# Performance work log

Hardware: AMD Instinct MI355X
Metric: run time of the kernel (lower is better)

## Reference

```python
import jax, jax.numpy as jnp
import numpy as np

M, NN, D, H, DFF, L, EPG = 128, 62, 512, 8, 2048, 4, 600
K1, K2 = 50, 40  # ceil(0.8*62), ceil(0.8*50)
EPS = 1e-5


def _ln(x, g, b):
    mu = x.mean(-1, keepdims=True)
    v = x.var(-1, keepdims=True)
    return (x - mu) * jax.lax.rsqrt(v + EPS) * g + b


def _gcn(x, src, dst, mask, W, b, n):
    # PyG GCNConv: add self-loops, sym-normalized scatter-add aggregation
    h = x @ W
    w = mask.astype(x.dtype)
    deg = 1.0 + jax.ops.segment_sum(w, dst, num_segments=n)  # +1 self-loop
    dis = jax.lax.rsqrt(deg)
    coef = dis[src] * w * dis[dst]
    agg = jax.ops.segment_sum(coef[:, None] * h[src], dst, num_segments=n)
    return agg + h * (dis * dis)[:, None] + b  # second term = self-loop message


def _sagpool(x, src, dst, mask, Ws, bs, m, n_per, k):
    n = m * n_per
    score = _gcn(x, src, dst, mask, Ws, bs, n)[:, 0]
    _, topi = jax.lax.top_k(score.reshape(m, n_per), k)  # per-graph topk
    perm = (topi + jnp.arange(m)[:, None] * n_per).reshape(-1)
    xn = x[perm] * jnp.tanh(score[perm])[:, None]
    # filter_adj: keep edges with both endpoints surviving, remap indices
    nmap = jnp.full((n,), -1, jnp.int32).at[perm].set(jnp.arange(m * k, dtype=jnp.int32))
    ns, nd = nmap[src], nmap[dst]
    keep = mask & (ns >= 0) & (nd >= 0)
    return xn, jnp.where(keep, ns, 0), jnp.where(keep, nd, 0), keep


def _enc_layer(x, Wqkv, bqkv, Wo, bo, W1, b1, W2, b2, g1, be1, g2, be2):
    # post-norm TransformerEncoderLayer, relu activation, eval (no dropout)
    S, B, Dm = x.shape
    dh = Dm // H
    q, k, v = jnp.split(x @ Wqkv + bqkv, 3, axis=-1)
    q = q.reshape(S, B, H, dh)
    k = k.reshape(S, B, H, dh)
    v = v.reshape(S, B, H, dh)
    att = jnp.einsum('sbhd,tbhd->bhst', q, k) * (1.0 / np.sqrt(dh))
    o = jnp.einsum('bhst,tbhd->sbhd', jax.nn.softmax(att, axis=-1), v).reshape(S, B, Dm)
    x = _ln(x + o @ Wo + bo, g1, be1)
    f = jax.nn.relu(x @ W1 + b1) @ W2 + b2
    return _ln(x + f, g2, be2)


def _readout(h, m, k):
    hr = h.reshape(m, k, -1)
    return jnp.concatenate([hr.max(axis=1), hr.mean(axis=1)], axis=-1)  # gmp||gap


def _forward(edge_index, x, bn_g, bn_b, W_emb, enc_Wqkv, enc_bqkv, enc_Wo, enc_bo, enc_W1, enc_b1, enc_W2, enc_b2, enc_g1, enc_be1, enc_g2, enc_be2, W_emb1, conv1_W, conv1_b, convs_W, convs_b, pool1_W, pool1_b, pool2_W, pool2_b, fc1_W, fc1_b, fc2_W, fc2_b, fc3_W, fc3_b):
    m = x.shape[0] // NN
    xr = x.reshape(m, NN, NN)
    # BatchNorm1d(62) in training mode: per-channel stats over (N, L)
    mu = xr.mean(axis=(0, 2), keepdims=True)
    var = xr.var(axis=(0, 2), keepdims=True)
    xb = (xr - mu) * jax.lax.rsqrt(var + EPS) * bn_g[None, :, None] + bn_b[None, :, None]
    t = xb.transpose(1, 0, 2) @ W_emb  # [62, m, D] seq-first
    for l in range(L):
        t = _enc_layer(t, enc_Wqkv[l], enc_bqkv[l], enc_Wo[l], enc_bo[l], enc_W1[l], enc_b1[l], enc_W2[l], enc_b2[l], enc_g1[l], enc_be1[l], enc_g2[l], enc_be2[l])
    # faithful to torch: reshape [62,m,62] directly to [m*62,62] (no permute back)
    xg = (t @ W_emb1).reshape(m * NN, NN)
    src, dst = edge_index[0], edge_index[1]
    mask0 = jnp.ones(src.shape, bool)
    h = jax.nn.relu(_gcn(xg, src, dst, mask0, conv1_W, conv1_b, m * NN))
    h, s1, d1, m1 = _sagpool(h, src, dst, mask0, pool1_W, pool1_b, m, NN, K1)
    x1 = _readout(h, m, K1)
    for l in range(L - 1):
        h = jax.nn.relu(_gcn(h, s1, d1, m1, convs_W[l], convs_b[l], m * K1))
    h, s2, d2, m2 = _sagpool(h, s1, d1, m1, pool2_W, pool2_b, m, K1, K2)
    x2 = _readout(h, m, K2)
    z = x1 + x2
    z = jax.nn.relu(z @ fc1_W + fc1_b)
    z = jax.nn.relu(z @ fc2_W + fc2_b)
    return z @ fc3_W + fc3_b


def setup_inputs():
    key = jax.random.key(0)
    ki = iter(jax.random.split(key, 40))
    def nrm(shape, s=0.05):
        return jax.random.normal(next(ki), shape, jnp.float32) * s
    x = jax.random.normal(next(ki), (M * NN, NN), jnp.float32)
    off = jnp.arange(M, dtype=jnp.int32)[:, None] * NN
    src = jax.random.randint(next(ki), (M, EPG), 0, NN, dtype=jnp.int32) + off
    dst = jax.random.randint(next(ki), (M, EPG), 0, NN, dtype=jnp.int32) + off
    edge_index = jnp.stack([src.reshape(-1), dst.reshape(-1)])
    return dict(
        x=x, edge_index=edge_index,
        bn_g=jnp.ones(NN), bn_b=jnp.zeros(NN),
        W_emb=nrm((NN, D)),
        enc_Wqkv=nrm((L, D, 3 * D)), enc_bqkv=jnp.zeros((L, 3 * D)),
        enc_Wo=nrm((L, D, D)), enc_bo=jnp.zeros((L, D)),
        enc_W1=nrm((L, D, DFF)), enc_b1=jnp.zeros((L, DFF)),
        enc_W2=nrm((L, DFF, D)), enc_b2=jnp.zeros((L, D)),
        enc_g1=jnp.ones((L, D)), enc_be1=jnp.zeros((L, D)),
        enc_g2=jnp.ones((L, D)), enc_be2=jnp.zeros((L, D)),
        W_emb1=nrm((D, NN)),
        conv1_W=nrm((NN, D)), conv1_b=jnp.zeros(D),
        convs_W=nrm((L - 1, D, D)), convs_b=jnp.zeros((L - 1, D)),
        pool1_W=nrm((D, 1)), pool1_b=jnp.zeros(1),
        pool2_W=nrm((D, 1)), pool2_b=jnp.zeros(1),
        fc1_W=nrm((2 * D, D)), fc1_b=jnp.zeros(D),
        fc2_W=nrm((D, D // 2)), fc2_b=jnp.zeros(D // 2),
        fc3_W=nrm((D // 2, 2)), fc3_b=jnp.zeros(2))


def reference(x, edge_index, bn_g, bn_b, W_emb, enc_Wqkv, enc_bqkv, enc_Wo, enc_bo, enc_W1, enc_b1, enc_W2, enc_b2, enc_g1, enc_be1, enc_g2, enc_be2, W_emb1, conv1_W, conv1_b, convs_W, convs_b, pool1_W, pool1_b, pool2_W, pool2_b, fc1_W, fc1_b, fc2_W, fc2_b, fc3_W, fc3_b):
    return _forward(edge_index, x, bn_g, bn_b, W_emb, enc_Wqkv, enc_bqkv, enc_Wo, enc_bo, enc_W1, enc_b1, enc_W2, enc_b2, enc_g1, enc_be1, enc_g2, enc_be2, W_emb1, conv1_W, conv1_b, convs_W, convs_b, pool1_W, pool1_b, pool2_W, pool2_b, fc1_W, fc1_b, fc2_W, fc2_b, fc3_W, fc3_b)
```

## Files before the change

kernel.cpp:

```cpp
#include <hip/hip_runtime.h>
#include <float.h>
#include <math.h>

#define MG 128
#define NNODE 62
#define DD 512
#define NH 8
#define DH 64
#define DFF 2048
#define NLAYER 4
#define EPG 600
#define KP1 50
#define KP2 40
#define NTOK (MG*NNODE)
#define NEDGE (MG*EPG)
#define EPSV 1e-5f

typedef unsigned short u16;
using bf16x8 = __attribute__((ext_vector_type(8))) short;
using f32x4  = __attribute__((ext_vector_type(4))) float;

__device__ __forceinline__ float wave_sum(float v) {
  for (int off = 32; off; off >>= 1) v += __shfl_xor(v, off);
  return v;
}
__device__ __forceinline__ float wave_max(float v) {
  for (int off = 32; off; off >>= 1) v = fmaxf(v, __shfl_xor(v, off));
  return v;
}
__device__ __forceinline__ u16 f2b(float x) {
  union { float f; unsigned u; } v; v.f = x;
  unsigned r = v.u + 0x7fffu + ((v.u >> 16) & 1u);
  return (u16)(r >> 16);
}
__device__ __forceinline__ float b2f(u16 h) {
  union { float f; unsigned u; } v; v.u = ((unsigned)h) << 16;
  return v.f;
}
__device__ __forceinline__ void f2bsplit(float x, u16& h, u16& l) {
  h = f2b(x);
  l = f2b(x - b2f(h));
}
__device__ __forceinline__ void load_lds16(const u16* g, u16* l) {
  __builtin_amdgcn_global_load_lds(
      (const __attribute__((address_space(1))) unsigned int*)(const void*)g,
      (__attribute__((address_space(3))) unsigned int*)(void*)l, 16, 0, 0);
}

__global__ __launch_bounds__(256) void bn_stats_kernel(const float* __restrict__ x,
    float* __restrict__ mu, float* __restrict__ rs) {
  int s = blockIdx.x;
  float sum = 0.f, sq = 0.f;
  for (int i = threadIdx.x; i < MG*NNODE; i += 256) {
    int b = i / NNODE, j = i - b*NNODE;
    float v = x[(size_t)(b*NNODE + s)*NNODE + j];
    sum += v; sq += v*v;
  }
  __shared__ float r1[4], r2[4];
  sum = wave_sum(sum); sq = wave_sum(sq);
  int wv = threadIdx.x >> 6, lane = threadIdx.x & 63;
  if (lane == 0) { r1[wv] = sum; r2[wv] = sq; }
  __syncthreads();
  if (threadIdx.x == 0) {
    float S = r1[0]+r1[1]+r1[2]+r1[3];
    float Q = r2[0]+r2[1]+r2[2]+r2[3];
    float m = S / (float)(MG*NNODE);
    float var = Q / (float)(MG*NNODE) - m*m;
    mu[s] = m;
    rs[s] = rsqrtf(var + EPSV);
  }
}

__global__ __launch_bounds__(256) void embed_kernel(const float* __restrict__ x,
    const float* __restrict__ mu, const float* __restrict__ rs,
    const float* __restrict__ gg, const float* __restrict__ bb,
    const float* __restrict__ W, float* __restrict__ T,
    u16* __restrict__ Th, u16* __restrict__ Tl) {
  int tok = blockIdx.x;
  int s = tok >> 7, b = tok & 127;
  __shared__ float xb[NNODE];
  if (threadIdx.x < NNODE) {
    float v = x[(size_t)(b*NNODE + s)*NNODE + threadIdx.x];
    xb[threadIdx.x] = (v - mu[s]) * rs[s] * gg[s] + bb[s];
  }
  __syncthreads();
  int d = threadIdx.x;
  float a0 = 0.f, a1 = 0.f;
  for (int j = 0; j < NNODE; ++j) {
    float xv = xb[j];
    a0 += xv * W[(size_t)j*DD + d];
    a1 += xv * W[(size_t)j*DD + d + 256];
  }
  size_t o = (size_t)tok*DD + d;
  T[o] = a0; T[o+256] = a1;
  u16 h, l;
  f2bsplit(a0, h, l); Th[o] = h; Tl[o] = l;
  f2bsplit(a1, h, l); Th[o+256] = h; Tl[o+256] = l;
}

__global__ __launch_bounds__(256) void gemm_kernel(const float* __restrict__ A,
    const float* __restrict__ B, float* __restrict__ C, int M, int N, int K) {
  __shared__ float As[16][68];
  __shared__ float Bs[16][68];
  int bm = blockIdx.y * 64, bn = blockIdx.x * 64;
  int tid = threadIdx.x;
  int tx = tid & 15, ty = tid >> 4;
  float acc[4][4] = {};
  for (int k0 = 0; k0 < K; k0 += 16) {
    {
      int row = tid >> 2; int kk = (tid & 3) * 4;
      int gm = bm + row;
      #pragma unroll
      for (int i = 0; i < 4; ++i) {
        int gk = k0 + kk + i;
        As[kk+i][row] = (gm < M && gk < K) ? A[(size_t)gm*K + gk] : 0.f;
      }
    }
    {
      int krow = tid >> 4; int nn = (tid & 15) * 4;
      int gk = k0 + krow;
      #pragma unroll
      for (int i = 0; i < 4; ++i) {
        int gn = bn + nn + i;
        Bs[krow][nn+i] = (gk < K && gn < N) ? B[(size_t)gk*N + gn] : 0.f;
      }
    }
    __syncthreads();
    #pragma unroll
    for (int k = 0; k < 16; ++k) {
      float a[4], bb2[4];
      #pragma unroll
      for (int i = 0; i < 4; ++i) a[i] = As[k][ty*4+i];
      #pragma unroll
      for (int j = 0; j < 4; ++j) bb2[j] = Bs[k][tx*4+j];
      #pragma unroll
      for (int i = 0; i < 4; ++i)
        #pragma unroll
        for (int j = 0; j < 4; ++j) acc[i][j] += a[i]*bb2[j];
    }
    __syncthreads();
  }
  #pragma unroll
  for (int i = 0; i < 4; ++i) {
    int gm = bm + ty*4 + i;
    if (gm >= M) continue;
    #pragma unroll
    for (int j = 0; j < 4; ++j) {
      int gn = bn + tx*4 + j;
      if (gn >= N) continue;
      C[(size_t)gm*N + gn] = acc[i][j];
    }
  }
}

__device__ __forceinline__ void transpose_split_tile(const float* __restrict__ W,
    u16* __restrict__ th, u16* __restrict__ tl,
    int K, int N, int Kp, int bx, int by, float (*t)[65]) {
  int k0 = by*64, n0 = bx*64;
  for (int i = threadIdx.x; i < 64*64; i += 256) {
    int r = i >> 6, c = i & 63;
    int gk = k0 + r, gn = n0 + c;
    t[r][c] = (gk < K && gn < N) ? W[(size_t)gk*N + gn] : 0.f;
  }
  __syncthreads();
  for (int i = threadIdx.x; i < 64*64; i += 256) {
    int r = i >> 6, c = i & 63;
    int gn = n0 + r, gk = k0 + c;
    u16 h, l; f2bsplit(t[c][r], h, l);
    th[(size_t)gn*Kp + gk] = h;
    tl[(size_t)gn*Kp + gk] = l;
  }
}

__global__ __launch_bounds__(256) void layerT_kernel(
    const float* __restrict__ Wqkv, const float* __restrict__ Wo,
    const float* __restrict__ W1, const float* __restrict__ W2,
    u16* WQh, u16* WQl, u16* WOh, u16* WOl,
    u16* W1h, u16* W1l, u16* W2h, u16* W2l) {
  __shared__ float t[64][65];
  int b = blockIdx.x;
  if (b < 192)      transpose_split_tile(Wqkv, WQh, WQl, 512, 1536, 512, b % 24, b / 24, t);
  else if (b < 256) { int q = b - 192; transpose_split_tile(Wo, WOh, WOl, 512, 512, 512, q % 8, q / 8, t); }
  else if (b < 512) { int q = b - 256; transpose_split_tile(W1, W1h, W1l, 512, 2048, 512, q % 32, q / 32, t); }
  else              { int q = b - 512; transpose_split_tile(W2, W2h, W2l, 2048, 512, 2048, q % 8, q / 8, t); }
}

__global__ __launch_bounds__(256) void gcnT_kernel(
    const float* __restrict__ WC, const float* __restrict__ convs_W,
    u16* CTh, u16* CTl, u16* CVh, u16* CVl) {
  __shared__ float t[64][65];
  int job = blockIdx.x >> 6, q = blockIdx.x & 63;
  int bx = q % 8, by = q / 8;
  if (job == 0) transpose_split_tile(WC, CTh, CTl, 512, 512, 512, bx, by, t);
  else {
    int l = job - 1;
    transpose_split_tile(convs_W + (size_t)l*DD*DD,
        CVh + (size_t)l*DD*DD, CVl + (size_t)l*DD*DD, 512, 512, 512, bx, by, t);
  }
}

template<bool RELU, int OUTMODE>
__global__ __launch_bounds__(256) void gemm3_kernel(
    const u16* __restrict__ Ah, const u16* __restrict__ Al,
    const u16* __restrict__ Bh, const u16* __restrict__ Bl,
    const float* __restrict__ bias,
    float* __restrict__ Cf, u16* __restrict__ Ch, u16* __restrict__ Cl,
    int Nreal, int Nstride, int Kp, int KC) {
  __shared__ alignas(16) u16 sA[2][2][4096];
  __shared__ alignas(16) u16 sB[2][2][4096];
  unsigned nx = gridDim.x, ny = gridDim.y;
  unsigned nwg = nx * ny * gridDim.z;
  unsigned lb = blockIdx.x + nx*(blockIdx.y + ny*blockIdx.z);
  unsigned swz = lb;
  if ((nwg & 7u) == 0u) {
    unsigned cpx = nwg >> 3;
    swz = (lb & 7u)*cpx + (lb >> 3);
  }
  unsigned bxi = swz % nx;
  unsigned rem = swz / nx;
  unsigned byi = rem % ny;
  unsigned bzi = rem / ny;
  int bm = byi * 128, bn = bxi * 128;
  int z = bzi;
  int tid = threadIdx.x;
  int wv = tid >> 6, lane = tid & 63;
  int wr = (wv >> 1) * 64, wc = (wv & 1) * 64;
  f32x4 acc[4][4];
  #pragma unroll
  for (int i = 0; i < 4; ++i)
    #pragma unroll
    for (int j = 0; j < 4; ++j) acc[i][j] = (f32x4){0.f,0.f,0.f,0.f};

  int r0 = tid >> 2;
  int lin = (tid & 3) * 8;
  int c0 = lin ^ (((r0 >> 1) & 3) << 3);
  int r1 = r0 + 64;
  int c1 = lin ^ (((r1 >> 1) & 3) << 3);
  int fr = lane & 15, fo = (lane >> 4) * 8;

  auto stage = [&](int k0, int bi) {
    size_t a0 = (size_t)(bm + r0)*Kp + k0 + c0;
    size_t a1 = (size_t)(bm + r1)*Kp + k0 + c1;
    size_t b0 = (size_t)(bn + r0)*Kp + k0 + c0;
    size_t b1 = (size_t)(bn + r1)*Kp + k0 + c1;
    load_lds16(Ah + a0, &sA[bi][0][tid*8]);
    load_lds16(Ah + a1, &sA[bi][0][2048 + tid*8]);
    load_lds16(Al + a0, &sA[bi][1][tid*8]);
    load_lds16(Al + a1, &sA[bi][1][2048 + tid*8]);
    load_lds16(Bh + b0, &sB[bi][0][tid*8]);
    load_lds16(Bh + b1, &sB[bi][0][2048 + tid*8]);
    load_lds16(Bl + b0, &sB[bi][1][tid*8]);
    load_lds16(Bl + b1, &sB[bi][1][2048 + tid*8]);
  };

  int kbeg = z * KC;
  int nk = KC >> 5;
  stage(kbeg, 0);
  __syncthreads();
  int cur = 0;
  for (int t = 0; t < nk; ++t) {
    if (t + 1 < nk) stage(kbeg + (t+1)*32, cur ^ 1);
    bf16x8 ah[4], al[4], bh[4], bl[4];
    #pragma unroll
    for (int i = 0; i < 4; ++i) {
      int ra = wr + i*16 + fr;
      int ea = ra*32 + (fo ^ (((ra >> 1) & 3) << 3));
      ah[i] = *(const bf16x8*)&sA[cur][0][ea];
      al[i] = *(const bf16x8*)&sA[cur][1][ea];
      int rb = wc + i*16 + fr;
      int eb = rb*32 + (fo ^ (((rb >> 1) & 3) << 3));
      bh[i] = *(const bf16x8*)&sB[cur][0][eb];
      bl[i] = *(const bf16x8*)&sB[cur][1][eb];
    }
    #pragma unroll
    for (int i = 0; i < 4; ++i)
      #pragma unroll
      for (int j = 0; j < 4; ++j) {
        acc[i][j] = __builtin_amdgcn_mfma_f32_16x16x32_bf16(ah[i], bh[j], acc[i][j], 0, 0, 0);
        acc[i][j] = __builtin_amdgcn_mfma_f32_16x16x32_bf16(ah[i], bl[j], acc[i][j], 0, 0, 0);
        acc[i][j] = __builtin_amdgcn_mfma_f32_16x16x32_bf16(al[i], bh[j], acc[i][j], 0, 0, 0);
      }
    __syncthreads();
    cur ^= 1;
  }
  size_t pstride = (size_t)gridDim.y * 128 * Nstride;
  int cr = (lane >> 4) * 4, cc = lane & 15;
  #pragma unroll
  for (int i = 0; i < 4; ++i) {
    #pragma unroll
    for (int j = 0; j < 4; ++j) {
      int gn = bn + wc + j*16 + cc;
      if (gn >= Nstride) continue;
      #pragma unroll
      for (int q = 0; q < 4; ++q) {
        int gm = bm + wr + i*16 + cr + q;
        float v = acc[i][j][q];
        if (gn < Nreal) { if (bias && z == 0) v += bias[gn]; } else v = 0.f;
        if (RELU) v = fmaxf(v, 0.f);
        size_t o = (size_t)z*pstride + (size_t)gm*Nstride + gn;
        if (OUTMODE == 0) {
          Cf[o] = v;
        } else {
          u16 h, l; f2bsplit(v, h, l);
          Ch[o] = h; Cl[o] = l;
        }
      }
    }
  }
}

__global__ __launch_bounds__(256) void attn_kernel(const float* __restrict__ QKV,
    u16* __restrict__ Oh, u16* __restrict__ Ol) {
  int b = blockIdx.x >> 3, h = blockIdx.x & 7;
  __shared__ float qs[NNODE][DH+1];
  __shared__ float ks[NNODE][DH+1];
  __shared__ float ps[NNODE][DH+1];
  for (int i = threadIdx.x; i < NNODE*DH; i += 256) {
    int s = i >> 6, d = i & 63;
    size_t base = ((size_t)(s*MG + b))*(3*DD) + h*DH + d;
    qs[s][d] = QKV[base];
    ks[s][d] = QKV[base + DD];
  }
  __syncthreads();
  int lane = threadIdx.x & 63, wv = threadIdx.x >> 6;
  for (int s = wv; s < NNODE; s += 4) {
    float acc = -FLT_MAX;
    if (lane < NNODE) {
      float a = 0.f;
      #pragma unroll
      for (int d = 0; d < DH; ++d) a += qs[s][d]*ks[lane][d];
      acc = a * 0.125f;
    }
    float mx = wave_max(acc);
    float e = (lane < NNODE) ? expf(acc - mx) : 0.f;
    float sm = wave_sum(e);
    ps[s][lane] = e / sm;
  }
  __syncthreads();
  for (int i = threadIdx.x; i < NNODE*DH; i += 256) {
    int s = i >> 6, d = i & 63;
    qs[s][d] = QKV[((size_t)(s*MG + b))*(3*DD) + 2*DD + h*DH + d];
  }
  __syncthreads();
  for (int s = wv; s < NNODE; s += 4) {
    float acc = 0.f;
    for (int t = 0; t < NNODE; ++t) acc += ps[s][t]*qs[t][lane];
    size_t o = ((size_t)(s*MG + b))*DD + h*DH + lane;
    u16 hh, ll; f2bsplit(acc, hh, ll);
    Oh[o] = hh; Ol[o] = ll;
  }
}

__global__ __launch_bounds__(256) void add_ln_kernel(float* __restrict__ X,
    const float* __restrict__ P, int nchunk,
    const float* __restrict__ gg, const float* __restrict__ bb,
    u16* __restrict__ Xh, u16* __restrict__ Xl) {
  size_t row = blockIdx.x;
  int t = threadIdx.x;
  const size_t MN = (size_t)NTOK*DD;
  float r0 = 0.f, r1 = 0.f;
  for (int z = 0; z < nchunk; ++z) {
    r0 += P[z*MN + row*DD + t];
    r1 += P[z*MN + row*DD + t + 256];
  }
  float v0 = X[row*DD + t] + r0;
  float v1 = X[row*DD + t + 256] + r1;
  __shared__ float red[4];
  float s = wave_sum(v0 + v1);
  int wv = t >> 6, lane = t & 63;
  if (lane == 0) red[wv] = s;
  __syncthreads();
  float mu = (red[0]+red[1]+red[2]+red[3]) * (1.f/DD);
  float d0 = v0 - mu, d1 = v1 - mu;
  float q = wave_sum(d0*d0 + d1*d1);
  __syncthreads();
  if (lane == 0) red[wv] = q;
  __syncthreads();
  float var = (red[0]+red[1]+red[2]+red[3]) * (1.f/DD);
  float rs = rsqrtf(var + EPSV);
  float o0 = d0*rs*gg[t] + bb[t];
  float o1 = d1*rs*gg[t+256] + bb[t+256];
  X[row*DD + t] = o0;
  X[row*DD + t+256] = o1;
  u16 h, l;
  f2bsplit(o0, h, l); Xh[row*DD + t] = h; Xl[row*DD + t] = l;
  f2bsplit(o1, h, l); Xh[row*DD + t+256] = h; Xl[row*DD + t+256] = l;
}

__global__ void fill_int_kernel(int* p, int v, int n) {
  int i = blockIdx.x*256 + threadIdx.x;
  if (i < n) p[i] = v;
}
__global__ void zero_f_kernel(float* p, int n) {
  int i = blockIdx.x*256 + threadIdx.x;
  if (i < n) p[i] = 0.f;
}
__global__ void count_deg_kernel(const int* __restrict__ dst, int* deg, int n) {
  int e = blockIdx.x*256 + threadIdx.x;
  if (e < n) atomicAdd(&deg[dst[e]], 1);
}
__global__ void dis_kernel(const int* __restrict__ deg, float* dis, int n) {
  int i = blockIdx.x*256+threadIdx.x;
  if (i < n) dis[i] = rsqrtf((float)deg[i]);
}
__global__ void coef0_kernel(const int* __restrict__ src, const int* __restrict__ dst,
                             const float* __restrict__ dis, float* coef) {
  int e = blockIdx.x*256+threadIdx.x;
  if (e < NEDGE) coef[e] = dis[src[e]]*dis[dst[e]];
}
__global__ void coef1_kernel(const int* __restrict__ src, const int* __restrict__ dst,
                             const int* __restrict__ keep,
                             const float* __restrict__ dis, float* coef) {
  int e = blockIdx.x*256+threadIdx.x;
  if (e < NEDGE) coef[e] = keep[e] ? dis[src[e]]*dis[dst[e]] : 0.f;
}

__global__ __launch_bounds__(64) void diagA_kernel(const float* __restrict__ dis,
    float* __restrict__ AG, int NP) {
  int g = blockIdx.x, lane = threadIdx.x;
  if (lane < NP) {
    float d = dis[g*NP + lane];
    AG[(size_t)g*4096 + lane*64 + lane] = d*d;
  }
}
__global__ __launch_bounds__(256) void edgeA_kernel(const int* __restrict__ src,
    const int* __restrict__ dst, const float* __restrict__ coef,
    float* __restrict__ AG, int NP) {
  int e = blockIdx.x*256 + threadIdx.x;
  if (e >= NEDGE) return;
  float c = coef[e];
  if (c == 0.f) return;
  int g = e / EPG;
  int ls = src[e] - g*NP, ld = dst[e] - g*NP;
  atomicAdd(&AG[(size_t)g*4096 + ld*64 + ls], c);
}

__global__ __launch_bounds__(256) void dense_agg_kernel(
    const float* __restrict__ AG,
    const float* __restrict__ P, int nchunk, size_t mn,
    const float* __restrict__ bias,
    float* __restrict__ Hout, int NP, int relu,
    u16* __restrict__ outh, u16* __restrict__ outl) {
  int g = blockIdx.x >> 3;
  int ct = (blockIdx.x & 7) * 64;
  __shared__ float hls[64*64];
  __shared__ float At[64*68];
  int base = g * NP;
  for (int idx = threadIdx.x; idx < 64*64; idx += 256) {
    int r = idx >> 6, c = idx & 63;
    float v = 0.f;
    if (r < NP) {
      for (int z = 0; z < nchunk; ++z)
        v += P[z*mn + (size_t)(base+r)*DD + ct + c];
    }
    hls[idx] = v;
    At[c*68 + r] = AG[(size_t)g*4096 + idx];
  }
  __syncthreads();
  int wv = threadIdx.x >> 6, lane = threadIdx.x & 63;
  int i0 = wv * 16;
  f32x4 acc[4];
  #pragma unroll
  for (int q = 0; q < 4; ++q) acc[q] = (f32x4){0.f,0.f,0.f,0.f};
  for (int j = 0; j < NP; ++j) {
    float hv = hls[j*64 + lane];
    const f32x4* ap = (const f32x4*)&At[j*68 + i0];
    f32x4 a0 = ap[0], a1 = ap[1], a2 = ap[2], a3 = ap[3];
    #pragma unroll
    for (int t = 0; t < 4; ++t) {
      acc[0][t] += a0[t] * hv;
      acc[1][t] += a1[t] * hv;
      acc[2][t] += a2[t] * hv;
      acc[3][t] += a3[t] * hv;
    }
  }
  float bv = bias[ct + lane];
  #pragma unroll
  for (int q = 0; q < 4; ++q) {
    #pragma unroll
    for (int t = 0; t < 4; ++t) {
      int i = i0 + q*4 + t;
      if (i < NP) {
        float v = acc[q][t] + bv;
        if (relu) v = fmaxf(v, 0.f);
        size_t o = (size_t)(base+i)*DD + ct + lane;
        Hout[o] = v;
        if (outh) { u16 h, l; f2bsplit(v, h, l); outh[o] = h; outl[o] = l; }
      }
    }
  }
}

__global__ __launch_bounds__(64) void dense_score_kernel(
    const float* __restrict__ AG, const float* __restrict__ hsv,
    const float* __restrict__ pb, float* __restrict__ sc, int NP) {
  int g = blockIdx.x, lane = threadIdx.x;
  __shared__ float hls[64];
  __shared__ float At[64*65];
  hls[lane] = (lane < NP) ? hsv[g*NP + lane] : 0.f;
  for (int idx = lane; idx < 64*64; idx += 64) {
    int i = idx >> 6, j = idx & 63;
    At[j*65 + i] = AG[(size_t)g*4096 + idx];
  }
  __syncthreads();
  if (lane < NP) {
    float acc = 0.f;
    for (int j = 0; j < NP; ++j) acc += At[j*65 + lane] * hls[j];
    sc[g*NP + lane] = acc + pb[0];
  }
}

__global__ __launch_bounds__(256) void gemv_kernel(const float* __restrict__ h,
    const float* __restrict__ wv, float* __restrict__ out, int n) {
  int node = blockIdx.x*4 + (threadIdx.x >> 6);
  int lane = threadIdx.x & 63;
  if (node >= n) return;
  const float* row = h + (size_t)node*DD;
  float acc = 0.f;
  for (int d = lane; d < DD; d += 64) acc += row[d]*wv[d];
  acc = wave_sum(acc);
  if (lane == 0) out[node] = acc;
}

__global__ __launch_bounds__(64) void topk_kernel(const float* __restrict__ sc,
    int* __restrict__ perm, int NP, int KK) {
  int g = blockIdx.x, lane = threadIdx.x;
  float v = (lane < NP) ? sc[g*NP+lane] : -FLT_MAX;
  for (int r = 0; r < KK; ++r) {
    float bv = v; int bi = lane;
    for (int off = 32; off; off >>= 1) {
      float ov = __shfl_xor(bv, off);
      int oi = __shfl_xor(bi, off);
      if (ov > bv || (ov == bv && oi < bi)) { bv = ov; bi = oi; }
    }
    if (lane == 0) perm[g*KK + r] = bi;
    if (lane == bi) v = -FLT_MAX;
  }
}

__global__ __launch_bounds__(256) void gather_kernel(const float* __restrict__ h,
    const float* __restrict__ sc, const int* __restrict__ perm,
    float* __restrict__ xn, u16* __restrict__ outh, u16* __restrict__ outl,
    int NP, int KK) {
  int j = blockIdx.x;
  int g = j / KK;
  int pi = perm[j];
  float t = tanhf(sc[g*NP + pi]);
  const float* srow = h + (size_t)(g*NP + pi)*DD;
  size_t o = (size_t)j*DD + threadIdx.x;
  float v0 = srow[threadIdx.x]*t;
  float v1 = srow[threadIdx.x+256]*t;
  xn[o] = v0; xn[o+256] = v1;
  if (outh) {
    u16 hh, ll;
    f2bsplit(v0, hh, ll); outh[o] = hh; outl[o] = ll;
    f2bsplit(v1, hh, ll); outh[o+256] = hh; outl[o+256] = ll;
  }
}

__global__ void nmap_scatter_kernel(const int* __restrict__ perm, int* __restrict__ nmap) {
  int j = blockIdx.x*256 + threadIdx.x;
  if (j < MG*KP1) nmap[(j/KP1)*NNODE + perm[j]] = j;
}

__global__ void filter_kernel(const int* __restrict__ src0, const int* __restrict__ dst0,
    const int* __restrict__ nmap, int* __restrict__ es, int* __restrict__ ed,
    int* __restrict__ keep, int* __restrict__ deg1) {
  int e = blockIdx.x*256+threadIdx.x;
  if (e >= NEDGE) return;
  int ns = nmap[src0[e]], nd = nmap[dst0[e]];
  int k = (ns >= 0) && (nd >= 0);
  es[e] = k ? ns : 0;
  ed[e] = k ? nd : 0;
  keep[e] = k;
  if (k) atomicAdd(&deg1[nd], 1);
}

__global__ __launch_bounds__(256) void readout_kernel(const float* __restrict__ h,
    float* __restrict__ z, int KK, int acc) {
  int g = blockIdx.x;
  for (int c = threadIdx.x; c < DD; c += 256) {
    float mx = -FLT_MAX, sm = 0.f;
    for (int r = 0; r < KK; ++r) {
      float v = h[(size_t)(g*KK+r)*DD + c];
      mx = fmaxf(mx, v); sm += v;
    }
    float mean = sm / (float)KK;
    if (acc) { z[(size_t)g*1024 + c] += mx; z[(size_t)g*1024 + 512 + c] += mean; }
    else     { z[(size_t)g*1024 + c]  = mx; z[(size_t)g*1024 + 512 + c]  = mean; }
  }
}

__global__ __launch_bounds__(256) void mlp1_kernel(const float* __restrict__ Z,
    const float* __restrict__ W1, float* __restrict__ Pm) {
  int b = blockIdx.x;
  int g = b >> 2, zc = b & 3;
  __shared__ float z[256];
  int t = threadIdx.x;
  z[t] = Z[(size_t)g*1024 + zc*256 + t];
  __syncthreads();
  const float* Wb = W1 + (size_t)zc*256*512;
  float a0 = 0.f, a1 = 0.f;
  for (int k = 0; k < 256; ++k) {
    float zv = z[k];
    a0 += zv * Wb[(size_t)k*512 + t];
    a1 += zv * Wb[(size_t)k*512 + t + 256];
  }
  size_t o = ((size_t)zc*MG + g)*512;
  Pm[o + t] = a0;
  Pm[o + t + 256] = a1;
}

__global__ __launch_bounds__(256) void mlp2_kernel(const float* __restrict__ Pm,
    const float* __restrict__ b1,
    const float* __restrict__ W2, const float* __restrict__ b2,
    const float* __restrict__ W3, const float* __restrict__ b3,
    float* __restrict__ out) {
  int g = blockIdx.x;
  int t = threadIdx.x;
  int wv = t >> 6, lane = t & 63;
  __shared__ float h1[512];
  __shared__ float p2[4][256];
  __shared__ float h2[256];
  #pragma unroll
  for (int half = 0; half < 2; ++half) {
    int n = t + half*256;
    float a = b1[n];
    #pragma unroll
    for (int zc = 0; zc < 4; ++zc) a += Pm[((size_t)zc*MG + g)*512 + n];
    h1[n] = fmaxf(a, 0.f);
  }
  __syncthreads();
  {
    float a[4] = {0.f, 0.f, 0.f, 0.f};
    for (int k = wv*128; k < wv*128 + 128; ++k) {
      float hv = h1[k];
      #pragma unroll
      for (int q = 0; q < 4; ++q)
        a[q] += hv * W2[(size_t)k*256 + lane + q*64];
    }
    #pragma unroll
    for (int q = 0; q < 4; ++q) p2[wv][lane + q*64] = a[q];
  }
  __syncthreads();
  h2[t] = fmaxf(p2[0][t] + p2[1][t] + p2[2][t] + p2[3][t] + b2[t], 0.f);
  __syncthreads();
  if (wv < 2) {
    float acc = 0.f;
    for (int k = lane; k < 256; k += 64) acc += h2[k]*W3[(size_t)k*2 + wv];
    acc = wave_sum(acc);
    if (lane == 0) out[(size_t)g*2 + wv] = acc + b3[wv];
  }
}

extern "C" void kernel_launch(void* const* d_in, const int* in_sizes, int n_in,
                              void* d_out, int out_size, void* d_ws, size_t ws_size,
                              hipStream_t stream) {
  const float* x       = (const float*)d_in[0];
  const int*   edge    = (const int*)d_in[1];
  const float* bn_g    = (const float*)d_in[2];
  const float* bn_b    = (const float*)d_in[3];
  const float* W_emb   = (const float*)d_in[4];
  const float* Wqkv    = (const float*)d_in[5];
  const float* bqkv    = (const float*)d_in[6];
  const float* Wo      = (const float*)d_in[7];
  const float* bo      = (const float*)d_in[8];
  const float* W1      = (const float*)d_in[9];
  const float* b1      = (const float*)d_in[10];
  const float* W2      = (const float*)d_in[11];
  const float* b2      = (const float*)d_in[12];
  const float* g1      = (const float*)d_in[13];
  const float* be1     = (const float*)d_in[14];
  const float* g2      = (const float*)d_in[15];
  const float* be2     = (const float*)d_in[16];
  const float* W_emb1  = (const float*)d_in[17];
  const float* conv1_W = (const float*)d_in[18];
  const float* conv1_b = (const float*)d_in[19];
  const float* convs_W = (const float*)d_in[20];
  const float* convs_b = (const float*)d_in[21];
  const float* pool1_W = (const float*)d_in[22];
  const float* pool1_b = (const float*)d_in[23];
  const float* pool2_W = (const float*)d_in[24];
  const float* pool2_b = (const float*)d_in[25];
  const float* fc1_W   = (const float*)d_in[26];
  const float* fc1_b   = (const float*)d_in[27];
  const float* fc2_W   = (const float*)d_in[28];
  const float* fc2_b   = (const float*)d_in[29];
  const float* fc3_W   = (const float*)d_in[30];
  const float* fc3_b   = (const float*)d_in[31];
  (void)in_sizes; (void)n_in; (void)out_size; (void)ws_size;

  const int* srcp = edge;
  const int* dstp = edge + NEDGE;

  char* wsb = (char*)d_ws;
  size_t off = 0;
  auto alloc = [&](size_t bytes)->void* {
    void* p = wsb + off;
    off += (bytes + 255) & ~(size_t)255;
    return p;
  };
  const size_t MN = (size_t)NTOK*DD;
  float* T    = (float*)alloc(MN*4);
  size_t qkvB = (size_t)NTOK*3*DD*4, ffnB = (size_t)NTOK*DFF*2*2;
  char* BIGU  = (char*)alloc(qkvB > ffnB ? qkvB : ffnB);
  float* QKVf = (float*)BIGU;
  u16* BIGh   = (u16*)BIGU;
  u16* BIGl   = BIGh + (size_t)NTOK*DFF;
  float* PART = (float*)alloc(4*MN*4);
  u16* Th   = (u16*)alloc(MN*2);
  u16* Tl   = (u16*)alloc(MN*2);
  u16* ATh  = (u16*)alloc(MN*2);
  u16* ATl  = (u16*)alloc(MN*2);
  u16* Hh   = (u16*)alloc((size_t)MG*KP1*DD*2);
  u16* Hl   = (u16*)alloc((size_t)MG*KP1*DD*2);
  u16* WQh  = (u16*)alloc((size_t)1536*512*2);
  u16* WQl  = (u16*)alloc((size_t)1536*512*2);
  u16* WOh  = (u16*)alloc((size_t)512*512*2);
  u16* WOl  = (u16*)alloc((size_t)512*512*2);
  u16* W1h  = (u16*)alloc((size_t)2048*512*2);
  u16* W1l  = (u16*)alloc((size_t)2048*512*2);
  u16* W2h  = (u16*)alloc((size_t)512*2048*2);
  u16* W2l  = (u16*)alloc((size_t)512*2048*2);
  float* WCf = (float*)alloc((size_t)512*512*4);
  u16* CTh  = (u16*)alloc((size_t)512*512*2);
  u16* CTl  = (u16*)alloc((size_t)512*512*2);
  u16* CVh  = (u16*)alloc((size_t)3*512*512*2);
  u16* CVl  = (u16*)alloc((size_t)3*512*512*2);
  float* AG0 = (float*)alloc((size_t)MG*4096*4);
  float* AG1 = (float*)alloc((size_t)MG*4096*4);
  float* MU   = (float*)alloc(NNODE*4);
  float* RS   = (float*)alloc(NNODE*4);
  int*   DEG0 = (int*)alloc(NTOK*4);
  float* DIS0 = (float*)alloc(NTOK*4);
  float* COEF0= (float*)alloc(NEDGE*4);
  float* HS   = (float*)alloc(NTOK*4);
  float* SC   = (float*)alloc(NTOK*4);
  int*   PERM1= (int*)alloc(MG*KP1*4);
  int*   NMAP = (int*)alloc(NTOK*4);
  int*   ES1  = (int*)alloc(NEDGE*4);
  int*   ED1  = (int*)alloc(NEDGE*4);
  int*   KEEP1= (int*)alloc(NEDGE*4);
  int*   DEG1 = (int*)alloc(MG*KP1*4);
  float* DIS1 = (float*)alloc(MG*KP1*4);
  float* COEF1= (float*)alloc(NEDGE*4);
  int*   PERM2= (int*)alloc(MG*KP2*4);
  float* Z    = (float*)alloc(MG*1024*4);
  float* Pm   = (float*)alloc((size_t)4*MG*512*4);

  float* PA = PART;
  float* PB = PART + 2*MN;

  bn_stats_kernel<<<NNODE, 256, 0, stream>>>(x, MU, RS);
  embed_kernel<<<NTOK, 256, 0, stream>>>(x, MU, RS, bn_g, bn_b, W_emb, T, Th, Tl);
  fill_int_kernel<<<(NTOK+255)/256, 256, 0, stream>>>(DEG0, 1, NTOK);
  count_deg_kernel<<<(NEDGE+255)/256, 256, 0, stream>>>(dstp, DEG0, NEDGE);
  dis_kernel<<<(NTOK+255)/256, 256, 0, stream>>>(DEG0, DIS0, NTOK);
  coef0_kernel<<<(NEDGE+255)/256, 256, 0, stream>>>(srcp, dstp, DIS0, COEF0);
  zero_f_kernel<<<(MG*4096+255)/256, 256, 0, stream>>>(AG0, MG*4096);
  diagA_kernel<<<MG, 64, 0, stream>>>(DIS0, AG0, NNODE);
  edgeA_kernel<<<(NEDGE+255)/256, 256, 0, stream>>>(srcp, dstp, COEF0, AG0, NNODE);
  gemm_kernel<<<dim3(8,8), 256, 0, stream>>>(W_emb1, conv1_W, WCf, 512, 512, NNODE);
  gcnT_kernel<<<256, 256, 0, stream>>>(WCf, convs_W, CTh, CTl, CVh, CVl);

  for (int l = 0; l < NLAYER; ++l) {
    layerT_kernel<<<768, 256, 0, stream>>>(
        Wqkv + (size_t)l*DD*3*DD, Wo + (size_t)l*DD*DD,
        W1 + (size_t)l*DD*DFF, W2 + (size_t)l*DFF*DD,
        WQh, WQl, WOh, WOl, W1h, W1l, W2h, W2l);
    gemm3_kernel<false,0><<<dim3(12,62,1), 256, 0, stream>>>(Th, Tl, WQh, WQl,
        bqkv + (size_t)l*3*DD, QKVf, nullptr, nullptr, 3*DD, 3*DD, DD, DD);
    attn_kernel<<<MG*NH, 256, 0, stream>>>(QKVf, ATh, ATl);
    gemm3_kernel<false,0><<<dim3(4,62,2), 256, 0, stream>>>(ATh, ATl, WOh, WOl,
        bo + (size_t)l*DD, PART, nullptr, nullptr, DD, DD, DD, 256);
    add_ln_kernel<<<NTOK, 256, 0, stream>>>(T, PART, 2,
        g1 + (size_t)l*DD, be1 + (size_t)l*DD, Th, Tl);
    gemm3_kernel<true,1><<<dim3(16,62,1), 256, 0, stream>>>(Th, Tl, W1h, W1l,
        b1 + (size_t)l*DFF, nullptr, BIGh, BIGl, DFF, DFF, DD, DD);
    gemm3_kernel<false,0><<<dim3(4,62,2), 256, 0, stream>>>(BIGh, BIGl, W2h, W2l,
        b2 + (size_t)l*DD, PART, nullptr, nullptr, DD, DD, DFF, 1024);
    add_ln_kernel<<<NTOK, 256, 0, stream>>>(T, PART, 2,
        g2 + (size_t)l*DD, be2 + (size_t)l*DD, Th, Tl);
  }

  gemm3_kernel<false,0><<<dim3(4,62,2), 256, 0, stream>>>(Th, Tl, CTh, CTl,
      nullptr, PA, nullptr, nullptr, DD, DD, DD, 256);
  dense_agg_kernel<<<MG*8, 256, 0, stream>>>(AG0, PA, 2, MN, conv1_b,
      PA, NNODE, 1, nullptr, nullptr);

  gemv_kernel<<<(NTOK+3)/4, 256, 0, stream>>>(PA, pool1_W, HS, NTOK);
  dense_score_kernel<<<MG, 64, 0, stream>>>(AG0, HS, pool1_b, SC, NNODE);
  topk_kernel<<<MG, 64, 0, stream>>>(SC, PERM1, NNODE, KP1);
  gather_kernel<<<MG*KP1, 256, 0, stream>>>(PA, SC, PERM1, PA + MN, Hh, Hl, NNODE, KP1);
  readout_kernel<<<MG, 256, 0, stream>>>(PA + MN, Z, KP1, 0);

  fill_int_kernel<<<(NTOK+255)/256, 256, 0, stream>>>(NMAP, -1, NTOK);
  nmap_scatter_kernel<<<(MG*KP1+255)/256, 256, 0, stream>>>(PERM1, NMAP);
  fill_int_kernel<<<(MG*KP1+255)/256, 256, 0, stream>>>(DEG1, 1, MG*KP1);
  filter_kernel<<<(NEDGE+255)/256, 256, 0, stream>>>(srcp, dstp, NMAP, ES1, ED1, KEEP1, DEG1);
  dis_kernel<<<(MG*KP1+255)/256, 256, 0, stream>>>(DEG1, DIS1, MG*KP1);
  coef1_kernel<<<(NEDGE+255)/256, 256, 0, stream>>>(ES1, ED1, KEEP1, DIS1, COEF1);
  zero_f_kernel<<<(MG*4096+255)/256, 256, 0, stream>>>(AG1, MG*4096);
  diagA_kernel<<<MG, 64, 0, stream>>>(DIS1, AG1, KP1);
  edgeA_kernel<<<(NEDGE+255)/256, 256, 0, stream>>>(ES1, ED1, COEF1, AG1, KP1);

  const size_t MNP = (size_t)MG*KP1*DD;
  float* bases[3] = { PB, PA, PB };
  float* hfin = nullptr;
  for (int l = 0; l < NLAYER-1; ++l) {
    float* Pb = bases[l];
    gemm3_kernel<false,0><<<dim3(4,50,2), 256, 0, stream>>>(Hh, Hl, CVh + (size_t)l*DD*DD,
        CVl + (size_t)l*DD*DD, nullptr, Pb, nullptr, nullptr, DD, DD, DD, 256);
    dense_agg_kernel<<<MG*8, 256, 0, stream>>>(AG1, Pb, 2, MNP, convs_b + (size_t)l*DD,
        Pb, KP1, 1, (l < NLAYER-2) ? Hh : nullptr, (l < NLAYER-2) ? Hl : nullptr);
    hfin = Pb;
  }

  gemv_kernel<<<(MG*KP1+3)/4, 256, 0, stream>>>(hfin, pool2_W, HS, MG*KP1);
  dense_score_kernel<<<MG, 64, 0, stream>>>(AG1, HS, pool2_b, SC, KP1);
  topk_kernel<<<MG, 64, 0, stream>>>(SC, PERM2, KP1, KP2);
  gather_kernel<<<MG*KP2, 256, 0, stream>>>(hfin, SC, PERM2, PA, nullptr, nullptr, KP1, KP2);
  readout_kernel<<<MG, 256, 0, stream>>>(PA, Z, KP2, 1);

  mlp1_kernel<<<MG*4, 256, 0, stream>>>(Z, fc1_W, Pm);
  mlp2_kernel<<<MG, 256, 0, stream>>>(Pm, fc1_b, fc2_W, fc2_b, fc3_W, fc3_b, (float*)d_out);
}
```

Baseline: 1.808 ms.

## Overlap next-tile LDS staging with MFMA and write QKV in head-major layout

The GEMM main loop swaps __syncthreads for explicit s_waitcnt vmcnt(8) plus raw barriers. This lets the next tile's direct-to-LDS loads stay in flight while the current tile is computed, instead of draining all memory ops each iteration. Separately, the QKV projection gets a new output mode that scatters results into a [qkv][head][batch][seq][dh] layout. The attention kernel can then read Q/K/V contiguously instead of with a 3*512 stride. The cost is scattered stores in the GEMM epilogue, and the hand-tuned waitcnt relies on the exact count of 8 outstanding loads per stage.

```diff
diff --git a/kernel.cpp b/kernel.cpp
--- a/kernel.cpp
+++ b/kernel.cpp
@@ -256,10 +256,16 @@
   int kbeg = z * KC;
   int nk = KC >> 5;
   stage(kbeg, 0);
-  __syncthreads();
   int cur = 0;
   for (int t = 0; t < nk; ++t) {
-    if (t + 1 < nk) stage(kbeg + (t+1)*32, cur ^ 1);
+    if (t + 1 < nk) {
+      stage(kbeg + (t+1)*32, cur ^ 1);
+      asm volatile("s_waitcnt vmcnt(8)" ::: "memory");
+    } else {
+      asm volatile("s_waitcnt vmcnt(0)" ::: "memory");
+    }
+    __builtin_amdgcn_s_barrier();
+    __builtin_amdgcn_sched_barrier(0);
     bf16x8 ah[4], al[4], bh[4], bl[4];
     #pragma unroll
     for (int i = 0; i < 4; ++i) {
@@ -280,7 +286,7 @@
         acc[i][j] = __builtin_amdgcn_mfma_f32_16x16x32_bf16(ah[i], bl[j], acc[i][j], 0, 0, 0);
         acc[i][j] = __builtin_amdgcn_mfma_f32_16x16x32_bf16(al[i], bh[j], acc[i][j], 0, 0, 0);
       }
-    __syncthreads();
+    __builtin_amdgcn_s_barrier();
     cur ^= 1;
   }
   size_t pstride = (size_t)gridDim.y * 128 * Nstride;
@@ -297,12 +303,16 @@
         float v = acc[i][j][q];
         if (gn < Nreal) { if (bias && z == 0) v += bias[gn]; } else v = 0.f;
         if (RELU) v = fmaxf(v, 0.f);
-        size_t o = (size_t)z*pstride + (size_t)gm*Nstride + gn;
         if (OUTMODE == 0) {
-          Cf[o] = v;
-        } else {
+          Cf[(size_t)z*pstride + (size_t)gm*Nstride + gn] = v;
+        } else if (OUTMODE == 1) {
+          size_t o = (size_t)z*pstride + (size_t)gm*Nstride + gn;
           u16 h, l; f2bsplit(v, h, l);
           Ch[o] = h; Cl[o] = l;
+        } else {
+          int which = gn >> 9, hh2 = (gn >> 6) & 7, d = gn & 63;
+          int b2 = gm & 127, s2 = gm >> 7;
+          Cf[(size_t)((which*NH + hh2)*MG + b2)*(NNODE*DH) + s2*DH + d] = v;
         }
       }
     }
@@ -315,11 +325,12 @@
   __shared__ float qs[NNODE][DH+1];
   __shared__ float ks[NNODE][DH+1];
   __shared__ float ps[NNODE][DH+1];
+  size_t qb = (size_t)((0*NH + h)*MG + b)*(NNODE*DH);
+  size_t kb = (size_t)((1*NH + h)*MG + b)*(NNODE*DH);
+  size_t vb = (size_t)((2*NH + h)*MG + b)*(NNODE*DH);
   for (int i = threadIdx.x; i < NNODE*DH; i += 256) {
-    int s = i >> 6, d = i & 63;
-    size_t base = ((size_t)(s*MG + b))*(3*DD) + h*DH + d;
-    qs[s][d] = QKV[base];
-    ks[s][d] = QKV[base + DD];
+    qs[i >> 6][i & 63] = QKV[qb + i];
+    ks[i >> 6][i & 63] = QKV[kb + i];
   }
   __syncthreads();
   int lane = threadIdx.x & 63, wv = threadIdx.x >> 6;
@@ -338,8 +349,7 @@
   }
   __syncthreads();
   for (int i = threadIdx.x; i < NNODE*DH; i += 256) {
-    int s = i >> 6, d = i & 63;
-    qs[s][d] = QKV[((size_t)(s*MG + b))*(3*DD) + 2*DD + h*DH + d];
+    qs[i >> 6][i & 63] = QKV[vb + i];
   }
   __syncthreads();
   for (int s = wv; s < NNODE; s += 4) {
@@ -768,7 +778,7 @@
         Wqkv + (size_t)l*DD*3*DD, Wo + (size_t)l*DD*DD,
         W1 + (size_t)l*DD*DFF, W2 + (size_t)l*DFF*DD,
         WQh, WQl, WOh, WOl, W1h, W1l, W2h, W2l);
-    gemm3_kernel<false,0><<<dim3(12,62,1), 256, 0, stream>>>(Th, Tl, WQh, WQl,
+    gemm3_kernel<false,2><<<dim3(12,62,1), 256, 0, stream>>>(Th, Tl, WQh, WQl,
         bqkv + (size_t)l*3*DD, QKVf, nullptr, nullptr, 3*DD, 3*DD, DD, DD);
     attn_kernel<<<MG*NH, 256, 0, stream>>>(QKVf, ATh, ATl);
     gemm3_kernel<false,0><<<dim3(4,62,2), 256, 0, stream>>>(ATh, ATl, WOh, WOl,
```

Measured after the change: 1.801 ms. No clear change (-0.4%).
